# Performance work log

Measured on AMD Instinct MI355X. Metric: run time of the kernel, lower is better.

## Reference

```python
import jax, jax.numpy as jnp
from jax import lax
import numpy as np

BINS = 256

def setup_inputs() -> dict:
    key = jax.random.key(0)
    k1, k2 = jax.random.split(key)
    B, C, H, W = 8, 3, 1024, 1024
    dst = jax.random.uniform(k1, (B, C, H, W), dtype=jnp.float32)
    ref = jax.random.uniform(k2, (B, C, H, W), dtype=jnp.float32)
    return {"dst": dst, "ref": ref}


def _cal_hist(img):
    # img: [B,C,H,W] in [0,1]. torch.histc(img*255, bins=256, min=0, max=255):
    # bin width = 255/256, so bin = floor(img*255 / (255/256)) = floor(img*256).
    # Inputs are in [0,1) so nothing is out of histc's range (clip is a no-op safeguard).
    B, C, H, W = img.shape
    bc = B * C
    x = img.reshape(bc, H * W)
    idx = jnp.clip(jnp.floor(x * float(BINS)).astype(jnp.int32), 0, BINS - 1)
    rows = jnp.arange(bc, dtype=jnp.int32)[:, None]
    counts = jnp.zeros((bc, BINS), jnp.float32).at[rows, idx].add(1.0)
    # F.normalize(p=1, dim=1) with eps=1e-12
    counts = counts / jnp.maximum(jnp.sum(counts, axis=1, keepdims=True), 1e-12)
    # triu-bmm == cumulative sum -> per-channel CDF
    return jnp.cumsum(counts, axis=1)


def _trans_row(cdf_dst, cdf_ref):
    # Faithful vectorization of the sequential two-pointer loop in cal_trans.
    # For each i (pointer j only ever advances): match at the smallest
    # j' >= j with cdf_ref[j'-1] <= d <= cdf_ref[j']; if impossible, j runs
    # off to 256 and this and all later entries become 255.
    def step(j, d):
        s = jnp.searchsorted(cdf_ref, d)            # smallest s with cdf_ref[s] >= d, in [0,256]
        cand = jnp.maximum(j, s)                    # pointer never moves backwards; cand in [1,256]
        ok = (j < BINS) & (cand <= BINS - 1) & (d >= cdf_ref[cand - 1])
        out = jnp.where(ok, cand, BINS - 1)
        j_next = jnp.where(ok, cand, jnp.int32(BINS))
        return j_next, out.astype(jnp.int32)
    _, tail = lax.scan(step, jnp.int32(1), cdf_dst[1:])  # i = 1..255
    table = jnp.concatenate([jnp.zeros(1, jnp.int32), tail])  # table[0] = arange init = 0
    return table.at[BINS - 1].set(BINS - 1)                   # table[:,255] = 255


def reference(dst, ref):
    B, C, H, W = dst.shape
    bc = B * C
    hist_dst = _cal_hist(dst)   # [BC,256] CDFs
    hist_ref = _cal_hist(ref)
    tables = jax.vmap(_trans_row)(hist_dst, hist_ref)  # [BC,256] int32
    # NOTE: original code indexes tables[b*c] (not b*C+c) -- bug preserved faithfully.
    b_idx = jnp.arange(B, dtype=jnp.int32)[:, None]
    c_idx = jnp.arange(C, dtype=jnp.int32)[None, :]
    row_sel = (b_idx * c_idx).reshape(-1)               # [BC]
    luts = tables[row_sel]                              # [BC,256]
    pix = jnp.clip((dst * 255.0).astype(jnp.int32), 0, BINS - 1).reshape(bc, H * W)
    rst = jnp.take_along_axis(luts, pix, axis=1).reshape(B, C, H, W)
    return rst.astype(dst.dtype) / 255.0
```

## Files before the change

kernel.cpp:

```cpp
#include <hip/hip_runtime.h>

#define BINS 256
#define BC_N 24
#define C_N  3
#define NROWS 12
#define CH   64

__global__ __launch_bounds__(256) void hm_hist(const float* __restrict__ dst,
                                               const float* __restrict__ refp,
                                               unsigned int* __restrict__ part,
                                               int n4_per_row) {
    __shared__ unsigned int shist[BINS];
    __shared__ unsigned int wsum[2][BINS];

    const int t = threadIdx.x;
    const int l = t & 63;
    const int w = t >> 6;

    shist[t] = 0u;
    wsum[0][t] = 0u; wsum[1][t] = 0u;
    __syncthreads();

    const int y = blockIdx.y;
    const int row = (y < 9) ? y : 2 * y - 8;
    const float* img = blockIdx.z ? refp : dst;
    const int span = n4_per_row / CH;
    const float4* p = reinterpret_cast<const float4*>(img)
                    + (size_t)row * n4_per_row + (size_t)blockIdx.x * span;

    const int nsl = span >> 6;
    const int NA  = (nsl * 9) >> 4;

    if (w < 2) {
        for (int s = w; s < NA; s += 2) {
            float4 v = p[(s << 6) + l];
            atomicAdd(&shist[min((int)(v.x * 256.0f), BINS - 1)], 1u);
            atomicAdd(&shist[min((int)(v.y * 256.0f), BINS - 1)], 1u);
            atomicAdd(&shist[min((int)(v.z * 256.0f), BINS - 1)], 1u);
            atomicAdd(&shist[min((int)(v.w * 256.0f), BINS - 1)], 1u);
        }
        if (w == 0) {
            for (int j = (nsl << 6) + l; j < span; j += 64) {
                float4 v = p[j];
                atomicAdd(&shist[min((int)(v.x * 256.0f), BINS - 1)], 1u);
                atomicAdd(&shist[min((int)(v.y * 256.0f), BINS - 1)], 1u);
                atomicAdd(&shist[min((int)(v.z * 256.0f), BINS - 1)], 1u);
                atomicAdd(&shist[min((int)(v.w * 256.0f), BINS - 1)], 1u);
            }
            if (blockIdx.x == CH - 1) {
                for (int j = CH * span + l; j < n4_per_row; j += 64) {
                    const float4* pr = reinterpret_cast<const float4*>(img)
                                     + (size_t)row * n4_per_row;
                    float4 v = pr[j];
                    atomicAdd(&shist[min((int)(v.x * 256.0f), BINS - 1)], 1u);
                    atomicAdd(&shist[min((int)(v.y * 256.0f), BINS - 1)], 1u);
                    atomicAdd(&shist[min((int)(v.z * 256.0f), BINS - 1)], 1u);
                    atomicAdd(&shist[min((int)(v.w * 256.0f), BINS - 1)], 1u);
                }
            }
        }
    } else {
        const unsigned long long t0 = (l & 1)  ? 0ull : ~0ull;
        const unsigned long long t1 = (l & 2)  ? 0ull : ~0ull;
        const unsigned long long t2 = (l & 4)  ? 0ull : ~0ull;
        const unsigned long long t3 = (l & 8)  ? 0ull : ~0ull;
        const unsigned long long t4 = (l & 16) ? 0ull : ~0ull;
        const unsigned long long t5 = (l & 32) ? 0ull : ~0ull;
        unsigned int c0 = 0, c1 = 0, c2 = 0, c3 = 0;

        auto grp = [&](float x) {
            int bin = min((int)(x * 256.0f), BINS - 1);
            unsigned long long B0 = __ballot(bin & 1);
            unsigned long long B1 = __ballot(bin & 2);
            unsigned long long B2 = __ballot(bin & 4);
            unsigned long long B3 = __ballot(bin & 8);
            unsigned long long B4 = __ballot(bin & 16);
            unsigned long long B5 = __ballot(bin & 32);
            unsigned long long B6 = __ballot(bin & 64);
            unsigned long long B7 = __ballot(bin & 128);
            unsigned long long m = (B0 ^ t0) & (B1 ^ t1) & (B2 ^ t2)
                                 & (B3 ^ t3) & (B4 ^ t4) & (B5 ^ t5);
            unsigned long long a = m & ~B7, b = m & B7;
            c0 += (unsigned)__popcll(a & ~B6);
            c1 += (unsigned)__popcll(a &  B6);
            c2 += (unsigned)__popcll(b & ~B6);
            c3 += (unsigned)__popcll(b &  B6);
        };

        int s = NA + (w - 2);
        if (s < nsl) {
            float4 v = p[(s << 6) + l];
            for (; s + 2 < nsl; s += 2) {
                float4 nv = p[((s + 2) << 6) + l];
                __builtin_amdgcn_sched_barrier(0);
                grp(v.x); grp(v.y); grp(v.z); grp(v.w);
                v = nv;
            }
            grp(v.x); grp(v.y); grp(v.z); grp(v.w);
        }
        wsum[w - 2][l]       = c0;
        wsum[w - 2][l + 64]  = c1;
        wsum[w - 2][l + 128] = c2;
        wsum[w - 2][l + 192] = c3;
    }
    __syncthreads();

    unsigned int sv = shist[t] + wsum[0][t] + wsum[1][t];
    part[(((size_t)blockIdx.z * NROWS + y) * CH + blockIdx.x) * BINS + t] = sv;
}

__global__ __launch_bounds__(256) void hm_table(const unsigned int* __restrict__ part,
                                                float* __restrict__ lut) {
    __shared__ unsigned int sd[BINS], sr[BINS];
    __shared__ float cdf_d[BINS], cdf_r[BINS];
    __shared__ int firstFail;

    const int r = blockIdx.x;
    const int t = threadIdx.x;

    const unsigned int* pd = part + ((size_t)0 * NROWS + r) * CH * BINS;
    const unsigned int* pr = part + ((size_t)1 * NROWS + r) * CH * BINS;
    unsigned int xd = 0, xr = 0;
    #pragma unroll 8
    for (int k = 0; k < CH; ++k) {
        xd += pd[k * BINS + t];
        xr += pr[k * BINS + t];
    }
    if (t == 0) firstFail = BINS;
    sd[t] = xd; sr[t] = xr;
    __syncthreads();

    #pragma unroll
    for (int off = 1; off < BINS; off <<= 1) {
        unsigned int yd = (t >= off) ? sd[t - off] : 0u;
        unsigned int yr = (t >= off) ? sr[t - off] : 0u;
        __syncthreads();
        xd += yd; xr += yr;
        sd[t] = xd; sr[t] = xr;
        __syncthreads();
    }
    float totd = fmaxf((float)sd[BINS - 1], 1e-12f);
    float totr = fmaxf((float)sr[BINS - 1], 1e-12f);
    cdf_d[t] = (float)xd / totd;
    cdf_r[t] = (float)xr / totr;
    __syncthreads();

    int out;
    if (t == 0) {
        out = 0;
    } else {
        float d = cdf_d[t];
        int lo = 0, hi = BINS;
        while (lo < hi) {
            int m = (lo + hi) >> 1;
            if (cdf_r[m] < d) lo = m + 1; else hi = m;
        }
        int cand = lo > 1 ? lo : 1;
        bool ok = (cand <= BINS - 1) && (d >= cdf_r[cand - 1]);
        if (!ok) atomicMin(&firstFail, t);
        out = cand;
    }
    __syncthreads();

    if (t >= firstFail) out = BINS - 1;
    if (t == BINS - 1) out = BINS - 1;
    lut[(size_t)r * BINS + t] = (float)out / 255.0f;
}

__global__ __launch_bounds__(256) void hm_apply(const float* __restrict__ dst,
                                                const float* __restrict__ lut,
                                                float* __restrict__ out,
                                                int n4_per_row) {
    __shared__ float slut[BINS];
    const int bc = blockIdx.y;
    const int b = bc / C_N;
    const int c = bc - b * C_N;
    const int r = b * c;
    const int cr = (r <= 8) ? r : 8 + ((r - 8) >> 1);
    const int t = threadIdx.x;

    slut[t] = lut[(size_t)cr * BINS + t];
    __syncthreads();

    const float4* in4 = reinterpret_cast<const float4*>(dst) + (size_t)bc * n4_per_row;
    float4* out4 = reinterpret_cast<float4*>(out) + (size_t)bc * n4_per_row;
    const int gsz = gridDim.x * blockDim.x;

    #pragma unroll 4
    for (int i = blockIdx.x * blockDim.x + t; i < n4_per_row; i += gsz) {
        float4 v = in4[i];
        float4 o;
        o.x = slut[min(max((int)(v.x * 255.0f), 0), BINS - 1)];
        o.y = slut[min(max((int)(v.y * 255.0f), 0), BINS - 1)];
        o.z = slut[min(max((int)(v.z * 255.0f), 0), BINS - 1)];
        o.w = slut[min(max((int)(v.w * 255.0f), 0), BINS - 1)];
        out4[i] = o;
    }
}

extern "C" void kernel_launch(void* const* d_in, const int* in_sizes, int n_in,
                              void* d_out, int out_size, void* d_ws, size_t ws_size,
                              hipStream_t stream) {
    const float* dst  = (const float*)d_in[0];
    const float* refp = (const float*)d_in[1];
    float* out = (float*)d_out;

    const int total = in_sizes[0];
    const int hw = total / BC_N;
    const int n4 = hw >> 2;

    unsigned int* part = (unsigned int*)d_ws;
    float* lut = (float*)((char*)d_ws + (size_t)2 * NROWS * CH * BINS * sizeof(unsigned int));

    dim3 hg(CH, NROWS, 2);
    hm_hist<<<hg, dim3(256), 0, stream>>>(dst, refp, part, n4);

    hm_table<<<dim3(NROWS), dim3(256), 0, stream>>>(part, lut);

    dim3 ag(64, BC_N);
    hm_apply<<<ag, dim3(256), 0, stream>>>(dst, lut, out, n4);
}
```

Baseline: 71.89 us.

## Rebalance histogram waves into 512-thread blocks and unroll the apply loop

The histogram kernel moves to 512-thread blocks over half as many chunks per row. Five waves now use LDS atomics and three use ballot-based counting, with a retuned split ratio and a 3-deep load unroll. The apply kernel doubles its grid and processes two float4s per iteration, issuing both loads before the lookups. The aim is more memory-level parallelism and better latency hiding in these bandwidth-bound passes. In exchange, per-block LDS atomic contention rises and occupancy per CU changes.

```diff
diff --git a/kernel.cpp b/kernel.cpp
--- a/kernel.cpp
+++ b/kernel.cpp
@@ -4,21 +4,21 @@
 #define BC_N 24
 #define C_N  3
 #define NROWS 12
-#define CH   64
-
-__global__ __launch_bounds__(256) void hm_hist(const float* __restrict__ dst,
+#define CH   32
+#define ACH  128
+
+__global__ __launch_bounds__(512) void hm_hist(const float* __restrict__ dst,
                                                const float* __restrict__ refp,
                                                unsigned int* __restrict__ part,
                                                int n4_per_row) {
     __shared__ unsigned int shist[BINS];
-    __shared__ unsigned int wsum[2][BINS];
+    __shared__ unsigned int wsum[3][BINS];
 
     const int t = threadIdx.x;
     const int l = t & 63;
     const int w = t >> 6;
 
-    shist[t] = 0u;
-    wsum[0][t] = 0u; wsum[1][t] = 0u;
+    if (t < BINS) shist[t] = 0u;
     __syncthreads();
 
     const int y = blockIdx.y;
@@ -29,33 +29,55 @@
                     + (size_t)row * n4_per_row + (size_t)blockIdx.x * span;
 
     const int nsl = span >> 6;
-    const int NA  = (nsl * 9) >> 4;
-
-    if (w < 2) {
-        for (int s = w; s < NA; s += 2) {
+    const int na  = (nsl * 75) >> 7;
+
+    if (w < 5) {
+        const int per = na / 5;
+        const int rem = na - per * 5;
+        int s   = w * per + min(w, rem);
+        int cnt = per + (w < rem ? 1 : 0);
+        for (; cnt >= 3; cnt -= 3, s += 3) {
+            float4 v0 = p[((s + 0) << 6) + l];
+            float4 v1 = p[((s + 1) << 6) + l];
+            float4 v2 = p[((s + 2) << 6) + l];
+            __builtin_amdgcn_sched_barrier(0);
+            atomicAdd(&shist[min((int)(v0.x * 256.0f), 255)], 1u);
+            atomicAdd(&shist[min((int)(v0.y * 256.0f), 255)], 1u);
+            atomicAdd(&shist[min((int)(v0.z * 256.0f), 255)], 1u);
+            atomicAdd(&shist[min((int)(v0.w * 256.0f), 255)], 1u);
+            atomicAdd(&shist[min((int)(v1.x * 256.0f), 255)], 1u);
+            atomicAdd(&shist[min((int)(v1.y * 256.0f), 255)], 1u);
+            atomicAdd(&shist[min((int)(v1.z * 256.0f), 255)], 1u);
+            atomicAdd(&shist[min((int)(v1.w * 256.0f), 255)], 1u);
+            atomicAdd(&shist[min((int)(v2.x * 256.0f), 255)], 1u);
+            atomicAdd(&shist[min((int)(v2.y * 256.0f), 255)], 1u);
+            atomicAdd(&shist[min((int)(v2.z * 256.0f), 255)], 1u);
+            atomicAdd(&shist[min((int)(v2.w * 256.0f), 255)], 1u);
+        }
+        for (; cnt > 0; --cnt, ++s) {
             float4 v = p[(s << 6) + l];
-            atomicAdd(&shist[min((int)(v.x * 256.0f), BINS - 1)], 1u);
-            atomicAdd(&shist[min((int)(v.y * 256.0f), BINS - 1)], 1u);
-            atomicAdd(&shist[min((int)(v.z * 256.0f), BINS - 1)], 1u);
-            atomicAdd(&shist[min((int)(v.w * 256.0f), BINS - 1)], 1u);
+            atomicAdd(&shist[min((int)(v.x * 256.0f), 255)], 1u);
+            atomicAdd(&shist[min((int)(v.y * 256.0f), 255)], 1u);
+            atomicAdd(&shist[min((int)(v.z * 256.0f), 255)], 1u);
+            atomicAdd(&shist[min((int)(v.w * 256.0f), 255)], 1u);
         }
         if (w == 0) {
             for (int j = (nsl << 6) + l; j < span; j += 64) {
                 float4 v = p[j];
-                atomicAdd(&shist[min((int)(v.x * 256.0f), BINS - 1)], 1u);
-                atomicAdd(&shist[min((int)(v.y * 256.0f), BINS - 1)], 1u);
-                atomicAdd(&shist[min((int)(v.z * 256.0f), BINS - 1)], 1u);
-                atomicAdd(&shist[min((int)(v.w * 256.0f), BINS - 1)], 1u);
+                atomicAdd(&shist[min((int)(v.x * 256.0f), 255)], 1u);
+                atomicAdd(&shist[min((int)(v.y * 256.0f), 255)], 1u);
+                atomicAdd(&shist[min((int)(v.z * 256.0f), 255)], 1u);
+                atomicAdd(&shist[min((int)(v.w * 256.0f), 255)], 1u);
             }
             if (blockIdx.x == CH - 1) {
+                const float4* pr = reinterpret_cast<const float4*>(img)
+                                 + (size_t)row * n4_per_row;
                 for (int j = CH * span + l; j < n4_per_row; j += 64) {
-                    const float4* pr = reinterpret_cast<const float4*>(img)
-                                     + (size_t)row * n4_per_row;
                     float4 v = pr[j];
-                    atomicAdd(&shist[min((int)(v.x * 256.0f), BINS - 1)], 1u);
-                    atomicAdd(&shist[min((int)(v.y * 256.0f), BINS - 1)], 1u);
-                    atomicAdd(&shist[min((int)(v.z * 256.0f), BINS - 1)], 1u);
-                    atomicAdd(&shist[min((int)(v.w * 256.0f), BINS - 1)], 1u);
+                    atomicAdd(&shist[min((int)(v.x * 256.0f), 255)], 1u);
+                    atomicAdd(&shist[min((int)(v.y * 256.0f), 255)], 1u);
+                    atomicAdd(&shist[min((int)(v.z * 256.0f), 255)], 1u);
+                    atomicAdd(&shist[min((int)(v.w * 256.0f), 255)], 1u);
                 }
             }
         }
@@ -69,7 +91,7 @@
         unsigned int c0 = 0, c1 = 0, c2 = 0, c3 = 0;
 
         auto grp = [&](float x) {
-            int bin = min((int)(x * 256.0f), BINS - 1);
+            int bin = min((int)(x * 256.0f), 255);
             unsigned long long B0 = __ballot(bin & 1);
             unsigned long long B1 = __ballot(bin & 2);
             unsigned long long B2 = __ballot(bin & 4);
@@ -87,26 +109,28 @@
             c3 += (unsigned)__popcll(b &  B6);
         };
 
-        int s = NA + (w - 2);
+        int s = na + (w - 5);
         if (s < nsl) {
             float4 v = p[(s << 6) + l];
-            for (; s + 2 < nsl; s += 2) {
-                float4 nv = p[((s + 2) << 6) + l];
+            for (; s + 3 < nsl; s += 3) {
+                float4 nv = p[((s + 3) << 6) + l];
                 __builtin_amdgcn_sched_barrier(0);
                 grp(v.x); grp(v.y); grp(v.z); grp(v.w);
                 v = nv;
             }
             grp(v.x); grp(v.y); grp(v.z); grp(v.w);
         }
-        wsum[w - 2][l]       = c0;
-        wsum[w - 2][l + 64]  = c1;
-        wsum[w - 2][l + 128] = c2;
-        wsum[w - 2][l + 192] = c3;
-    }
-    __syncthreads();
-
-    unsigned int sv = shist[t] + wsum[0][t] + wsum[1][t];
-    part[(((size_t)blockIdx.z * NROWS + y) * CH + blockIdx.x) * BINS + t] = sv;
+        wsum[w - 5][l]       = c0;
+        wsum[w - 5][l + 64]  = c1;
+        wsum[w - 5][l + 128] = c2;
+        wsum[w - 5][l + 192] = c3;
+    }
+    __syncthreads();
+
+    if (t < BINS) {
+        unsigned int sv = shist[t] + wsum[0][t] + wsum[1][t] + wsum[2][t];
+        part[(((size_t)blockIdx.z * NROWS + y) * CH + blockIdx.x) * BINS + t] = sv;
+    }
 }
 
 __global__ __launch_bounds__(256) void hm_table(const unsigned int* __restrict__ part,
@@ -184,16 +208,32 @@
 
     const float4* in4 = reinterpret_cast<const float4*>(dst) + (size_t)bc * n4_per_row;
     float4* out4 = reinterpret_cast<float4*>(out) + (size_t)bc * n4_per_row;
-    const int gsz = gridDim.x * blockDim.x;
-
-    #pragma unroll 4
-    for (int i = blockIdx.x * blockDim.x + t; i < n4_per_row; i += gsz) {
+    const int gsz = gridDim.x * 256;
+
+    int i = blockIdx.x * 256 + t;
+    for (; i + gsz < n4_per_row; i += 2 * gsz) {
+        float4 v0 = in4[i];
+        float4 v1 = in4[i + gsz];
+        __builtin_amdgcn_sched_barrier(0);
+        float4 o0, o1;
+        o0.x = slut[min(max((int)(v0.x * 255.0f), 0), 255)];
+        o0.y = slut[min(max((int)(v0.y * 255.0f), 0), 255)];
+        o0.z = slut[min(max((int)(v0.z * 255.0f), 0), 255)];
+        o0.w = slut[min(max((int)(v0.w * 255.0f), 0), 255)];
+        o1.x = slut[min(max((int)(v1.x * 255.0f), 0), 255)];
+        o1.y = slut[min(max((int)(v1.y * 255.0f), 0), 255)];
+        o1.z = slut[min(max((int)(v1.z * 255.0f), 0), 255)];
+        o1.w = slut[min(max((int)(v1.w * 255.0f), 0), 255)];
+        out4[i] = o0;
+        out4[i + gsz] = o1;
+    }
+    for (; i < n4_per_row; i += gsz) {
         float4 v = in4[i];
         float4 o;
-        o.x = slut[min(max((int)(v.x * 255.0f), 0), BINS - 1)];
-        o.y = slut[min(max((int)(v.y * 255.0f), 0), BINS - 1)];
-        o.z = slut[min(max((int)(v.z * 255.0f), 0), BINS - 1)];
-        o.w = slut[min(max((int)(v.w * 255.0f), 0), BINS - 1)];
+        o.x = slut[min(max((int)(v.x * 255.0f), 0), 255)];
+        o.y = slut[min(max((int)(v.y * 255.0f), 0), 255)];
+        o.z = slut[min(max((int)(v.z * 255.0f), 0), 255)];
+        o.w = slut[min(max((int)(v.w * 255.0f), 0), 255)];
         out4[i] = o;
     }
 }
@@ -213,10 +253,10 @@
     float* lut = (float*)((char*)d_ws + (size_t)2 * NROWS * CH * BINS * sizeof(unsigned int));
 
     dim3 hg(CH, NROWS, 2);
-    hm_hist<<<hg, dim3(256), 0, stream>>>(dst, refp, part, n4);
+    hm_hist<<<hg, dim3(512), 0, stream>>>(dst, refp, part, n4);
 
     hm_table<<<dim3(NROWS), dim3(256), 0, stream>>>(part, lut);
 
-    dim3 ag(64, BC_N);
+    dim3 ag(ACH, BC_N);
     hm_apply<<<ag, dim3(256), 0, stream>>>(dst, lut, out, n4);
 }
```

Measured after the change: 70.05 us. 1.03x faster.
